# Optimization experiments

Measured on AMD Instinct MI355X. Metric: run time of the kernel, lower is better.

## Reference

```python
import jax, jax.numpy as jnp
import numpy as np

N, E, H = 100000, 3200000, 128


def setup_inputs() -> dict:
    key = jax.random.key(0)
    ks = jax.random.split(key, 12)
    s = 1.0 / np.sqrt(H)
    x = jax.random.normal(ks[0], (N, H), dtype=jnp.float32)
    edge_index = jax.random.randint(ks[1], (2, E), 0, N, dtype=jnp.int64)
    # GatedGraphConv weight: [num_layers=1, H, H] -> single [H, H]
    W = jax.random.normal(ks[2], (H, H), dtype=jnp.float32) * s
    # GRUCell (gate order: r, z, n)
    gru_w_ih = jax.random.normal(ks[3], (3 * H, H), dtype=jnp.float32) * s
    gru_w_hh = jax.random.normal(ks[4], (3 * H, H), dtype=jnp.float32) * s
    gru_b_ih = jax.random.normal(ks[5], (3 * H,), dtype=jnp.float32) * s
    gru_b_hh = jax.random.normal(ks[6], (3 * H,), dtype=jnp.float32) * s
    # LSTM layer 0 (gate order: i, f, g, o)
    lstm_w_ih = jax.random.normal(ks[7], (4 * H, H), dtype=jnp.float32) * s
    lstm_w_hh = jax.random.normal(ks[8], (4 * H, H), dtype=jnp.float32) * s
    lstm_b_ih = jax.random.normal(ks[9], (4 * H,), dtype=jnp.float32) * s
    lstm_b_hh = jax.random.normal(ks[10], (4 * H,), dtype=jnp.float32) * s
    return {
        "x": x, "edge_index": edge_index, "W": W,
        "gru_w_ih": gru_w_ih, "gru_w_hh": gru_w_hh,
        "gru_b_ih": gru_b_ih, "gru_b_hh": gru_b_hh,
        "lstm_w_ih": lstm_w_ih, "lstm_w_hh": lstm_w_hh,
        "lstm_b_ih": lstm_b_ih, "lstm_b_hh": lstm_b_hh,
    }


def _forward(x, edge_index, W, gru_w_ih, gru_w_hh, gru_b_ih, gru_b_hh,
             lstm_w_ih, lstm_w_hh, lstm_b_ih, lstm_b_hh):
    n = x.shape[0]
    src, dst = edge_index[0], edge_index[1]
    # GatedGraphConv, num_layers=1, mean aggregation
    m = x @ W                                   # [N, H]
    msg = m[src]                                # [E, H] gather (memory-bound)
    agg_sum = jax.ops.segment_sum(msg, dst, num_segments=n)
    deg = jax.ops.segment_sum(jnp.ones((src.shape[0],), x.dtype), dst, num_segments=n)
    agg = agg_sum / jnp.maximum(deg, 1.0)[:, None]
    # GRUCell(agg, x): gates r, z, n
    gi = agg @ gru_w_ih.T + gru_b_ih
    gh = x @ gru_w_hh.T + gru_b_hh
    i_r, i_z, i_n = jnp.split(gi, 3, axis=-1)
    h_r, h_z, h_n = jnp.split(gh, 3, axis=-1)
    r = jax.nn.sigmoid(i_r + h_r)
    z = jax.nn.sigmoid(i_z + h_z)
    ng = jnp.tanh(i_n + r * h_n)
    h_conv = (1.0 - z) * ng + z * x             # conv output H_tilde
    # 1-layer LSTM over seq_len=1 with zero initial (H, C)
    gates = h_conv @ lstm_w_ih.T + lstm_b_ih + lstm_b_hh  # h0 = 0
    i_g, f_g, g_g, o_g = jnp.split(gates, 4, axis=-1)
    c = jax.nn.sigmoid(i_g) * jnp.tanh(g_g)
    h_lstm = jax.nn.sigmoid(o_g) * jnp.tanh(c)
    return jax.nn.relu(h_lstm)


def reference(x, edge_index, W, gru_w_ih, gru_w_hh, gru_b_ih, gru_b_hh,
              lstm_w_ih, lstm_w_hh, lstm_b_ih, lstm_b_hh):
    return _forward(x, edge_index, W, gru_w_ih, gru_w_hh, gru_b_ih, gru_b_hh,
                    lstm_w_ih, lstm_w_hh, lstm_b_ih, lstm_b_hh)
```

## Files before the change

kernel.cpp:

```cpp
#include <hip/hip_runtime.h>
#include <math.h>

#define HD 128
#define PB 256
#define SCB 4096

typedef __attribute__((ext_vector_type(8))) short short8;
typedef __attribute__((ext_vector_type(4))) float f32x4;

__device__ __forceinline__ float sigf(float v) { return 1.0f / (1.0f + __expf(-v)); }

__device__ __forceinline__ unsigned short f2bf(float f) {
  union { float f; unsigned u; } v; v.f = f;
  unsigned r = (v.u + 0x7fffu + ((v.u >> 16) & 1u)) >> 16;
  return (unsigned short)r;
}
__device__ __forceinline__ float bf2f(unsigned short b) {
  union { unsigned u; float f; } v; v.u = ((unsigned)b) << 16;
  return v.f;
}


__global__ __launch_bounds__(256) void bcount_k(const int* __restrict__ ei,
                                                int* __restrict__ bcnt,
                                                int E, int N, int shift, int NB) {
  __shared__ int h[256];
  const int blk = blockIdx.x, tid = threadIdx.x;
  h[tid] = 0;
  __syncthreads();
  int per = (E + PB - 1) / PB;
  int lo = blk * per;
  int hi = (lo + per < E) ? lo + per : E;
  for (int e = lo + tid; e < hi; e += 256) {
    int d = ei[(size_t)E + e];
    if ((unsigned)d >= (unsigned)N) continue;
    atomicAdd(&h[d >> shift], 1);
  }
  __syncthreads();
  if (tid < NB) bcnt[tid * PB + blk] = h[tid];
}

__global__ __launch_bounds__(256) void scan1_k(const int* __restrict__ a,
                                               int* __restrict__ bsums, int total) {
  __shared__ int ts[256];
  int b = blockIdx.x, tid = threadIdx.x;
  int lo = b * SCB + tid * 16;
  int s = 0;
#pragma unroll
  for (int i = 0; i < 16; ++i) {
    int idx = lo + i;
    if (idx < total) s += a[idx];
  }
  ts[tid] = s;
  __syncthreads();
  for (int off = 128; off > 0; off >>= 1) {
    if (tid < off) ts[tid] += ts[tid + off];
    __syncthreads();
  }
  if (tid == 0) bsums[b] = ts[0];
}

__global__ __launch_bounds__(256) void scan2_k(int* __restrict__ bsums, int nb) {
  __shared__ int ts[256];
  int tid = threadIdx.x;
  int v = (tid < nb) ? bsums[tid] : 0;
  ts[tid] = v;
  __syncthreads();
  for (int off = 1; off < 256; off <<= 1) {
    int u = (tid >= off) ? ts[tid - off] : 0;
    __syncthreads();
    ts[tid] += u;
    __syncthreads();
  }
  if (tid < nb) bsums[tid] = ts[tid] - v;
}

__global__ __launch_bounds__(256) void scan3_k(int* __restrict__ a,
                                               const int* __restrict__ bsums,
                                               int total, int nblk) {
  __shared__ int ts[256];
  int b = blockIdx.x, tid = threadIdx.x;
  int lo = b * SCB + tid * 16;
  int pre[16];
  int s = 0;
#pragma unroll
  for (int i = 0; i < 16; ++i) {
    int idx = lo + i;
    int xv = (idx < total) ? a[idx] : 0;
    pre[i] = s;
    s += xv;
  }
  ts[tid] = s;
  __syncthreads();
  for (int off = 1; off < 256; off <<= 1) {
    int u = (tid >= off) ? ts[tid - off] : 0;
    __syncthreads();
    ts[tid] += u;
    __syncthreads();
  }
  int off0 = ts[tid] - s + bsums[b];
#pragma unroll
  for (int i = 0; i < 16; ++i) {
    int idx = lo + i;
    if (idx < total) a[idx] = off0 + pre[i];
  }
  if (b == nblk - 1 && tid == 255) a[total] = off0 + s;
}

__global__ __launch_bounds__(256) void bpart_k(const int* __restrict__ ei,
                                               const int* __restrict__ bstart,
                                               unsigned* __restrict__ ebuf,
                                               int E, int N, int shift, int NB,
                                               int sbits) {
  __shared__ int cur[256];
  const int blk = blockIdx.x, tid = threadIdx.x;
  if (tid < NB) cur[tid] = bstart[tid * PB + blk];
  __syncthreads();
  int per = (E + PB - 1) / PB;
  int lo = blk * per;
  int hi = (lo + per < E) ? lo + per : E;
  const unsigned dmask = (1u << shift) - 1u;
  for (int e = lo + tid; e < hi; e += 256) {
    int s = ei[e];
    int d = ei[(size_t)E + e];
    if ((unsigned)s >= (unsigned)N || (unsigned)d >= (unsigned)N) continue;
    int p = atomicAdd(&cur[d >> shift], 1);
    ebuf[p] = (((unsigned)d & dmask) << sbits) | (unsigned)s;
  }
}

__global__ __launch_bounds__(256) void bfill2_k(const unsigned* __restrict__ ebuf,
                                                const int* __restrict__ bstart,
                                                int* __restrict__ rowstart,
                                                int* __restrict__ csr,
                                                int N, int shift, int NB, int sbits) {
  __shared__ int cnt[2048];
  __shared__ int tsum[256];
  const int b = blockIdx.x, tid = threadIdx.x;
  const int d0 = b << shift;
  int dmax = d0 + (1 << shift);
  if (dmax > N) dmax = N;
  const int nd = dmax - d0;
  const unsigned smask = (1u << sbits) - 1u;
  for (int i = tid; i < nd; i += 256) cnt[i] = 0;
  __syncthreads();
  const int base = bstart[b * PB];
  const int end = bstart[(b + 1) * PB];
  for (int idx = base + tid; idx < end; idx += 256)
    atomicAdd(&cnt[ebuf[idx] >> sbits], 1);
  __syncthreads();
  const int C = (nd + 255) / 256;
  int lo = tid * C;
  int hi = (lo + C < nd) ? lo + C : nd;
  int loc[8];
  int s = 0;
  for (int i = lo; i < hi; ++i) {
    loc[i - lo] = cnt[i];
    s += cnt[i];
  }
  tsum[tid] = s;
  __syncthreads();
  for (int off = 1; off < 256; off <<= 1) {
    int u = (tid >= off) ? tsum[tid - off] : 0;
    __syncthreads();
    tsum[tid] += u;
    __syncthreads();
  }
  int run = tsum[tid] - s + base;
  for (int i = lo; i < hi; ++i) {
    rowstart[d0 + i] = run;
    cnt[i] = run;
    run += loc[i - lo];
  }
  if (b == NB - 1 && tid == 255) rowstart[N] = end;
  __syncthreads();
  for (int idx = base + tid; idx < end; idx += 256) {
    unsigned pk = ebuf[idx];
    int p = atomicAdd(&cnt[pk >> sbits], 1);
    csr[p] = (int)(pk & smask);
  }
}


__global__ __launch_bounds__(256) void convx_k(const float* __restrict__ x,
                                               unsigned short* __restrict__ xb, int n4) {
  int t = blockIdx.x * 256 + threadIdx.x;
  if (t >= n4) return;
  float4 v = reinterpret_cast<const float4*>(x)[t];
  ushort4 o;
  o.x = f2bf(v.x); o.y = f2bf(v.y); o.z = f2bf(v.z); o.w = f2bf(v.w);
  reinterpret_cast<ushort4*>(xb)[t] = o;
}

__global__ __launch_bounds__(256) void prepw_k(
    const float* __restrict__ gwhh, const float* __restrict__ lwih,
    const float* __restrict__ lbih, const float* __restrict__ lbhh,
    unsigned short* __restrict__ gwhhb, unsigned short* __restrict__ lwb,
    float* __restrict__ lbias) {
  int t = blockIdx.x * 256 + threadIdx.x;
  if (t < 49152) { gwhhb[t] = f2bf(gwhh[t]); return; }
  t -= 49152;
  if (t < 49152) {
    int j = t >> 7, k = t & 127;
    int jm = j < 128 ? j : j + 128;
    lwb[t] = f2bf(lwih[(size_t)jm * 128 + k]);
    return;
  }
  t -= 49152;
  if (t < 384) {
    int jm = t < 128 ? t : t + 128;
    lbias[t] = lbih[jm] + lbhh[jm];
  }
}

__global__ __launch_bounds__(256) void prepbp_k(const float* __restrict__ W,
                                                const float* __restrict__ gwih,
                                                unsigned short* __restrict__ Bpb) {
  int t = blockIdx.x * 256 + threadIdx.x;
  if (t >= 49152) return;
  int j = t >> 7, k = t & 127;
  const float4* wr = reinterpret_cast<const float4*>(W + (size_t)k * 128);
  const float4* gr = reinterpret_cast<const float4*>(gwih + (size_t)j * 128);
  float acc = 0.f;
#pragma unroll
  for (int c = 0; c < 32; ++c) {
    float4 a = wr[c], b = gr[c];
    acc += a.x * b.x + a.y * b.y + a.z * b.z + a.w * b.w;
  }
  Bpb[t] = f2bf(acc);
}

__device__ __forceinline__ void acc8(float* acc, uint4 v) {
  acc[0] += bf2f((unsigned short)v.x);
  acc[1] += bf2f((unsigned short)(v.x >> 16));
  acc[2] += bf2f((unsigned short)v.y);
  acc[3] += bf2f((unsigned short)(v.y >> 16));
  acc[4] += bf2f((unsigned short)v.z);
  acc[5] += bf2f((unsigned short)(v.z >> 16));
  acc[6] += bf2f((unsigned short)v.w);
  acc[7] += bf2f((unsigned short)(v.w >> 16));
}

__global__ __launch_bounds__(256) void gather_b_k(const int* __restrict__ csr,
                                                  const int* __restrict__ rowstart,
                                                  const unsigned short* __restrict__ xb,
                                                  unsigned short* __restrict__ xaggb, int N) {
  int w = (int)(((long long)blockIdx.x * 256 + threadIdx.x) >> 6);
  if (w >= N) return;
  const int lane = threadIdx.x & 63;
  const int sub = lane >> 4, li = lane & 15;
  const int beg = rowstart[w], end = rowstart[w + 1];
  const uint4* x4 = reinterpret_cast<const uint4*>(xb);

  float acc[8] = {0.f, 0.f, 0.f, 0.f, 0.f, 0.f, 0.f, 0.f};

  int j = beg;
  for (; j + 16 <= end; j += 16) {
    int s0 = csr[j + sub];
    int s1 = csr[j + 4 + sub];
    int s2 = csr[j + 8 + sub];
    int s3 = csr[j + 12 + sub];
    uint4 v0 = x4[(size_t)s0 * 16 + li];
    uint4 v1 = x4[(size_t)s1 * 16 + li];
    uint4 v2 = x4[(size_t)s2 * 16 + li];
    uint4 v3 = x4[(size_t)s3 * 16 + li];
    acc8(acc, v0); acc8(acc, v1); acc8(acc, v2); acc8(acc, v3);
  }
  for (; j + 4 <= end; j += 4) {
    int s0 = csr[j + sub];
    uint4 v0 = x4[(size_t)s0 * 16 + li];
    acc8(acc, v0);
  }
  int rem = end - j;
  if (sub < rem) {
    int s0 = csr[j + sub];
    uint4 v0 = x4[(size_t)s0 * 16 + li];
    acc8(acc, v0);
  }

#pragma unroll
  for (int i = 0; i < 8; ++i) {
    acc[i] += __shfl_xor(acc[i], 16, 64);
    acc[i] += __shfl_xor(acc[i], 32, 64);
  }

  if (lane < 16) {
    float scale = 1.0f / fmaxf((float)(end - beg), 1.0f);
    uint4 o;
    o.x = (unsigned)f2bf(acc[0] * scale) | ((unsigned)f2bf(acc[1] * scale) << 16);
    o.y = (unsigned)f2bf(acc[2] * scale) | ((unsigned)f2bf(acc[3] * scale) << 16);
    o.z = (unsigned)f2bf(acc[4] * scale) | ((unsigned)f2bf(acc[5] * scale) << 16);
    o.w = (unsigned)f2bf(acc[6] * scale) | ((unsigned)f2bf(acc[7] * scale) << 16);
    reinterpret_cast<uint4*>(xaggb)[(size_t)w * 16 + li] = o;
  }
}

__global__ __launch_bounds__(256) void gru_fused_k(
    const unsigned short* __restrict__ xaggb, const unsigned short* __restrict__ xb,
    const unsigned short* __restrict__ Bpb, const unsigned short* __restrict__ gwhhb,
    const float* __restrict__ gbih, const float* __restrict__ gbhh,
    unsigned short* __restrict__ hconv, int nrows) {
  __shared__ unsigned short Bsm[6][32][136];
  const int tid = threadIdx.x;
  const int w = tid >> 6, lane = tid & 63;
  const int q = lane >> 4, r = lane & 15;
  const int row0 = blockIdx.y * 64;
  const int c0 = blockIdx.x * 32;

#pragma unroll
  for (int it = 0; it < 12; ++it) {
    int idx = it * 256 + tid;
    int p = idx >> 9;
    int rem = idx & 511;
    int col = rem >> 4, kq = rem & 15;
    const unsigned short* src =
        (p < 3) ? Bpb + ((size_t)(p * 128 + c0 + col)) * HD
                : gwhhb + ((size_t)((p - 3) * 128 + c0 + col)) * HD;
    uint4 v = *reinterpret_cast<const uint4*>(src + kq * 8);
    *reinterpret_cast<uint4*>(&Bsm[p][col][kq * 8]) = v;
  }
  __syncthreads();

  int arow = row0 + (w << 4) + r;
  int ar = arow < nrows ? arow : nrows - 1;
  const unsigned short* Aa = xaggb + (size_t)ar * HD + q * 8;
  const unsigned short* Ax = xb + (size_t)ar * HD + q * 8;

  f32x4 acc[6][2];
#pragma unroll
  for (int p = 0; p < 6; ++p)
#pragma unroll
    for (int cb = 0; cb < 2; ++cb) acc[p][cb] = (f32x4)0.f;

#pragma unroll
  for (int ks = 0; ks < 4; ++ks) {
    short8 a1 = *reinterpret_cast<const short8*>(Aa + ks * 32);
    short8 a2 = *reinterpret_cast<const short8*>(Ax + ks * 32);
#pragma unroll
    for (int p = 0; p < 6; ++p) {
      short8 af = (p < 3) ? a1 : a2;
#pragma unroll
      for (int cb = 0; cb < 2; ++cb) {
        short8 bf = *reinterpret_cast<const short8*>(&Bsm[p][cb * 16 + r][ks * 32 + q * 8]);
        acc[p][cb] = __builtin_amdgcn_mfma_f32_16x16x32_bf16(af, bf, acc[p][cb], 0, 0, 0);
      }
    }
  }

#pragma unroll
  for (int cb = 0; cb < 2; ++cb) {
    int col = c0 + cb * 16 + r;
    float bir = gbih[col], biz = gbih[col + 128], bin = gbih[col + 256];
    float bhr = gbhh[col], bhz = gbhh[col + 128], bhn = gbhh[col + 256];
#pragma unroll
    for (int reg = 0; reg < 4; ++reg) {
      int row = row0 + (w << 4) + q * 4 + reg;
      if (row < nrows) {
        float ir = acc[0][cb][reg] + bir, iz = acc[1][cb][reg] + biz;
        float inn = acc[2][cb][reg] + bin;
        float hr = acc[3][cb][reg] + bhr, hz = acc[4][cb][reg] + bhz;
        float hn = acc[5][cb][reg] + bhn;
        float rr = sigf(ir + hr), zz = sigf(iz + hz);
        float nn = tanhf(inn + rr * hn);
        float xv = bf2f(xb[(size_t)row * HD + col]);
        hconv[(size_t)row * HD + col] = f2bf((1.f - zz) * nn + zz * xv);
      }
    }
  }
}

__global__ __launch_bounds__(256) void lstm_fused_k(
    const unsigned short* __restrict__ hconv, const unsigned short* __restrict__ lwb,
    const float* __restrict__ lbias, float* __restrict__ out, int nrows) {
  __shared__ unsigned short Bsm[3][64][136];
  const int tid = threadIdx.x;
  const int w = tid >> 6, lane = tid & 63;
  const int q = lane >> 4, r = lane & 15;
  const int row0 = blockIdx.y * 64;
  const int c0 = blockIdx.x * 64;

#pragma unroll
  for (int it = 0; it < 12; ++it) {
    int idx = it * 256 + tid;
    int p = idx >> 10, rem = idx & 1023;
    int col = rem >> 4, kq = rem & 15;
    uint4 v = *reinterpret_cast<const uint4*>(
        lwb + ((size_t)(p * 128 + c0 + col)) * HD + kq * 8);
    *reinterpret_cast<uint4*>(&Bsm[p][col][kq * 8]) = v;
  }
  __syncthreads();

  int arow = row0 + (w << 4) + r;
  int ar = arow < nrows ? arow : nrows - 1;
  const unsigned short* Ap = hconv + (size_t)ar * HD + q * 8;

  f32x4 acc[3][4];
#pragma unroll
  for (int p = 0; p < 3; ++p)
#pragma unroll
    for (int cb = 0; cb < 4; ++cb) acc[p][cb] = (f32x4)0.f;

#pragma unroll
  for (int ks = 0; ks < 4; ++ks) {
    short8 af = *reinterpret_cast<const short8*>(Ap + ks * 32);
#pragma unroll
    for (int p = 0; p < 3; ++p)
#pragma unroll
      for (int cb = 0; cb < 4; ++cb) {
        short8 bf = *reinterpret_cast<const short8*>(&Bsm[p][cb * 16 + r][ks * 32 + q * 8]);
        acc[p][cb] = __builtin_amdgcn_mfma_f32_16x16x32_bf16(af, bf, acc[p][cb], 0, 0, 0);
      }
  }

#pragma unroll
  for (int cb = 0; cb < 4; ++cb) {
    int col = c0 + cb * 16 + r;
    float bi = lbias[col], bg = lbias[col + 128], bo = lbias[col + 256];
#pragma unroll
    for (int reg = 0; reg < 4; ++reg) {
      int row = row0 + (w << 4) + q * 4 + reg;
      if (row < nrows) {
        float ig = acc[0][cb][reg] + bi;
        float gg = acc[1][cb][reg] + bg;
        float og = acc[2][cb][reg] + bo;
        float cc = sigf(ig) * tanhf(gg);
        out[(size_t)row * HD + col] = fmaxf(sigf(og) * tanhf(cc), 0.f);
      }
    }
  }
}


extern "C" void kernel_launch(void* const* d_in, const int* in_sizes, int n_in,
                              void* d_out, int out_size, void* d_ws, size_t ws_size,
                              hipStream_t stream) {
  const float* x = (const float*)d_in[0];
  const int* ei = (const int*)d_in[1];
  const float* W = (const float*)d_in[2];
  const float* gw_ih = (const float*)d_in[3];
  const float* gw_hh = (const float*)d_in[4];
  const float* gb_ih = (const float*)d_in[5];
  const float* gb_hh = (const float*)d_in[6];
  const float* lw_ih = (const float*)d_in[7];
  const float* lb_ih = (const float*)d_in[9];
  const float* lb_hh = (const float*)d_in[10];
  float* out = (float*)d_out;

  const int N = in_sizes[0] / HD;
  const int E = in_sizes[1] / 2;
  const size_t nH = (size_t)N * HD;

  int shift = 9;
  while (((N + (1 << shift) - 1) >> shift) > 256) ++shift;
  const int NB = (N + (1 << shift) - 1) >> shift;
  const int sbits = 32 - shift;

  const size_t N4p = (size_t)((N + 1 + 7) & ~7);
  const size_t E4 = (size_t)((E + 3) & ~3);
  const size_t BC = (size_t)NB * PB + 8;
  const int sc_total = NB * PB;
  const int sc_nblk = (sc_total + SCB - 1) / SCB;

  char* p = (char*)d_ws;
  int* rowstart = (int*)p;  p += 4 * N4p;
  int* bcnt = (int*)p;      p += 4 * BC;
  int* bsums = (int*)p;     p += 4 * 64;
  int* csr = (int*)p;       p += 4 * E4;
  size_t sz_eb = 4 * E4, sz_xb = 2 * nH;
  unsigned* ebuf = (unsigned*)p;
  unsigned short* xb = (unsigned short*)p;
  p += (sz_eb > sz_xb ? sz_eb : sz_xb);
  unsigned short* hconv = (unsigned short*)p;  p += 2 * nH;
  unsigned short* Bpb = (unsigned short*)p;    p += 2 * 49152;
  unsigned short* gwhhb = (unsigned short*)p;  p += 2 * 49152;
  unsigned short* lwb = (unsigned short*)p;    p += 2 * 49152;
  float* lbias = (float*)p;                    p += 4 * 384;

  unsigned short* xaggb = (unsigned short*)d_out;

  dim3 blk(256);
  unsigned rb = (unsigned)((N + 63) / 64);

  bcount_k<<<PB, blk, 0, stream>>>(ei, bcnt, E, N, shift, NB);
  scan1_k<<<sc_nblk, blk, 0, stream>>>(bcnt, bsums, sc_total);
  scan2_k<<<1, blk, 0, stream>>>(bsums, sc_nblk);
  scan3_k<<<sc_nblk, blk, 0, stream>>>(bcnt, bsums, sc_total, sc_nblk);
  bpart_k<<<PB, blk, 0, stream>>>(ei, bcnt, ebuf, E, N, shift, NB, sbits);
  bfill2_k<<<NB, blk, 0, stream>>>(ebuf, bcnt, rowstart, csr, N, shift, NB, sbits);

  convx_k<<<(unsigned)((nH / 4 + 255) / 256), blk, 0, stream>>>(x, xb, (int)(nH / 4));
  prepw_k<<<(2 * 49152 + 384 + 255) / 256, blk, 0, stream>>>(
      gw_hh, lw_ih, lb_ih, lb_hh, gwhhb, lwb, lbias);
  prepbp_k<<<192, blk, 0, stream>>>(W, gw_ih, Bpb);

  long long gthreads = (long long)N * 64;
  gather_b_k<<<(unsigned)((gthreads + 255) / 256), blk, 0, stream>>>(
      csr, rowstart, xb, xaggb, N);

  gru_fused_k<<<dim3(4, rb), blk, 0, stream>>>(
      xaggb, xb, Bpb, gwhhb, gb_ih, gb_hh, hconv, N);

  lstm_fused_k<<<dim3(2, rb), blk, 0, stream>>>(hconv, lwb, lbias, out, N);
}
```

Measured before the change: 500.2 us.

## Make GRU/LSTM GEMM kernels persistent and merge prep kernels into one launch

The GRU and LSTM fused GEMM kernels become persistent grid-stride loops over row tiles, with a capped grid of 512 blocks each. Each block loads its weight slice into shared memory and its biases once, then reuses them across many tiles instead of reloading them for every 64-row tile. The three preprocessing kernels (x conversion to bf16, weight conversion, and the W·W_ih product) are merged into a single launch to cut launch overhead. The trade-off is fewer blocks in flight, which may reduce the latency hiding available for the memory-bound A-row loads.

```diff
diff --git a/kernel.cpp b/kernel.cpp
--- a/kernel.cpp
+++ b/kernel.cpp
@@ -181,23 +181,22 @@
   }
 }
 
-
-__global__ __launch_bounds__(256) void convx_k(const float* __restrict__ x,
-                                               unsigned short* __restrict__ xb, int n4) {
-  int t = blockIdx.x * 256 + threadIdx.x;
-  if (t >= n4) return;
-  float4 v = reinterpret_cast<const float4*>(x)[t];
-  ushort4 o;
-  o.x = f2bf(v.x); o.y = f2bf(v.y); o.z = f2bf(v.z); o.w = f2bf(v.w);
-  reinterpret_cast<ushort4*>(xb)[t] = o;
-}
-
-__global__ __launch_bounds__(256) void prepw_k(
+__global__ __launch_bounds__(256) void prep_all_k(
+    const float* __restrict__ x, unsigned short* __restrict__ xb, int n4,
     const float* __restrict__ gwhh, const float* __restrict__ lwih,
     const float* __restrict__ lbih, const float* __restrict__ lbhh,
+    const float* __restrict__ W, const float* __restrict__ gwih,
     unsigned short* __restrict__ gwhhb, unsigned short* __restrict__ lwb,
-    float* __restrict__ lbias) {
+    float* __restrict__ lbias, unsigned short* __restrict__ Bpb) {
   int t = blockIdx.x * 256 + threadIdx.x;
+  if (t < n4) {
+    float4 v = reinterpret_cast<const float4*>(x)[t];
+    ushort4 o;
+    o.x = f2bf(v.x); o.y = f2bf(v.y); o.z = f2bf(v.z); o.w = f2bf(v.w);
+    reinterpret_cast<ushort4*>(xb)[t] = o;
+    return;
+  }
+  t -= n4;
   if (t < 49152) { gwhhb[t] = f2bf(gwhh[t]); return; }
   t -= 49152;
   if (t < 49152) {
@@ -210,24 +209,21 @@
   if (t < 384) {
     int jm = t < 128 ? t : t + 128;
     lbias[t] = lbih[jm] + lbhh[jm];
-  }
-}
-
-__global__ __launch_bounds__(256) void prepbp_k(const float* __restrict__ W,
-                                                const float* __restrict__ gwih,
-                                                unsigned short* __restrict__ Bpb) {
-  int t = blockIdx.x * 256 + threadIdx.x;
-  if (t >= 49152) return;
-  int j = t >> 7, k = t & 127;
-  const float4* wr = reinterpret_cast<const float4*>(W + (size_t)k * 128);
-  const float4* gr = reinterpret_cast<const float4*>(gwih + (size_t)j * 128);
-  float acc = 0.f;
-#pragma unroll
-  for (int c = 0; c < 32; ++c) {
-    float4 a = wr[c], b = gr[c];
-    acc += a.x * b.x + a.y * b.y + a.z * b.z + a.w * b.w;
-  }
-  Bpb[t] = f2bf(acc);
+    return;
+  }
+  t -= 384;
+  if (t < 49152) {
+    int j = t >> 7, k = t & 127;
+    const float4* wr = reinterpret_cast<const float4*>(W + (size_t)k * 128);
+    const float4* gr = reinterpret_cast<const float4*>(gwih + (size_t)j * 128);
+    float acc = 0.f;
+#pragma unroll
+    for (int c = 0; c < 32; ++c) {
+      float4 a = wr[c], b = gr[c];
+      acc += a.x * b.x + a.y * b.y + a.z * b.z + a.w * b.w;
+    }
+    Bpb[t] = f2bf(acc);
+  }
 }
 
 __device__ __forceinline__ void acc8(float* acc, uint4 v) {
@@ -304,7 +300,6 @@
   const int tid = threadIdx.x;
   const int w = tid >> 6, lane = tid & 63;
   const int q = lane >> 4, r = lane & 15;
-  const int row0 = blockIdx.y * 64;
   const int c0 = blockIdx.x * 32;
 
 #pragma unroll
@@ -321,49 +316,59 @@
   }
   __syncthreads();
 
-  int arow = row0 + (w << 4) + r;
-  int ar = arow < nrows ? arow : nrows - 1;
-  const unsigned short* Aa = xaggb + (size_t)ar * HD + q * 8;
-  const unsigned short* Ax = xb + (size_t)ar * HD + q * 8;
-
-  f32x4 acc[6][2];
-#pragma unroll
-  for (int p = 0; p < 6; ++p)
-#pragma unroll
-    for (int cb = 0; cb < 2; ++cb) acc[p][cb] = (f32x4)0.f;
-
-#pragma unroll
-  for (int ks = 0; ks < 4; ++ks) {
-    short8 a1 = *reinterpret_cast<const short8*>(Aa + ks * 32);
-    short8 a2 = *reinterpret_cast<const short8*>(Ax + ks * 32);
-#pragma unroll
-    for (int p = 0; p < 6; ++p) {
-      short8 af = (p < 3) ? a1 : a2;
-#pragma unroll
-      for (int cb = 0; cb < 2; ++cb) {
-        short8 bf = *reinterpret_cast<const short8*>(&Bsm[p][cb * 16 + r][ks * 32 + q * 8]);
-        acc[p][cb] = __builtin_amdgcn_mfma_f32_16x16x32_bf16(af, bf, acc[p][cb], 0, 0, 0);
+  float bir[2], biz[2], bin[2], bhr[2], bhz[2], bhn[2];
+#pragma unroll
+  for (int cb = 0; cb < 2; ++cb) {
+    int col = c0 + cb * 16 + r;
+    bir[cb] = gbih[col]; biz[cb] = gbih[col + 128]; bin[cb] = gbih[col + 256];
+    bhr[cb] = gbhh[col]; bhz[cb] = gbhh[col + 128]; bhn[cb] = gbhh[col + 256];
+  }
+
+  const int ntiles = (nrows + 63) >> 6;
+  for (int tile = blockIdx.y; tile < ntiles; tile += gridDim.y) {
+    const int row0 = tile << 6;
+    int arow = row0 + (w << 4) + r;
+    int ar = arow < nrows ? arow : nrows - 1;
+    const unsigned short* Aa = xaggb + (size_t)ar * HD + q * 8;
+    const unsigned short* Ax = xb + (size_t)ar * HD + q * 8;
+
+    f32x4 acc[6][2];
+#pragma unroll
+    for (int p = 0; p < 6; ++p)
+#pragma unroll
+      for (int cb = 0; cb < 2; ++cb) acc[p][cb] = (f32x4)0.f;
+
+#pragma unroll
+    for (int ks = 0; ks < 4; ++ks) {
+      short8 a1 = *reinterpret_cast<const short8*>(Aa + ks * 32);
+      short8 a2 = *reinterpret_cast<const short8*>(Ax + ks * 32);
+#pragma unroll
+      for (int p = 0; p < 6; ++p) {
+        short8 af = (p < 3) ? a1 : a2;
+#pragma unroll
+        for (int cb = 0; cb < 2; ++cb) {
+          short8 bf = *reinterpret_cast<const short8*>(&Bsm[p][cb * 16 + r][ks * 32 + q * 8]);
+          acc[p][cb] = __builtin_amdgcn_mfma_f32_16x16x32_bf16(af, bf, acc[p][cb], 0, 0, 0);
+        }
       }
     }
-  }
-
-#pragma unroll
-  for (int cb = 0; cb < 2; ++cb) {
-    int col = c0 + cb * 16 + r;
-    float bir = gbih[col], biz = gbih[col + 128], bin = gbih[col + 256];
-    float bhr = gbhh[col], bhz = gbhh[col + 128], bhn = gbhh[col + 256];
-#pragma unroll
-    for (int reg = 0; reg < 4; ++reg) {
-      int row = row0 + (w << 4) + q * 4 + reg;
-      if (row < nrows) {
-        float ir = acc[0][cb][reg] + bir, iz = acc[1][cb][reg] + biz;
-        float inn = acc[2][cb][reg] + bin;
-        float hr = acc[3][cb][reg] + bhr, hz = acc[4][cb][reg] + bhz;
-        float hn = acc[5][cb][reg] + bhn;
-        float rr = sigf(ir + hr), zz = sigf(iz + hz);
-        float nn = tanhf(inn + rr * hn);
-        float xv = bf2f(xb[(size_t)row * HD + col]);
-        hconv[(size_t)row * HD + col] = f2bf((1.f - zz) * nn + zz * xv);
+
+#pragma unroll
+    for (int cb = 0; cb < 2; ++cb) {
+      int col = c0 + cb * 16 + r;
+#pragma unroll
+      for (int reg = 0; reg < 4; ++reg) {
+        int row = row0 + (w << 4) + q * 4 + reg;
+        if (row < nrows) {
+          float ir = acc[0][cb][reg] + bir[cb], iz = acc[1][cb][reg] + biz[cb];
+          float inn = acc[2][cb][reg] + bin[cb];
+          float hr = acc[3][cb][reg] + bhr[cb], hz = acc[4][cb][reg] + bhz[cb];
+          float hn = acc[5][cb][reg] + bhn[cb];
+          float rr = sigf(ir + hr), zz = sigf(iz + hz);
+          float nn = tanhf(inn + rr * hn);
+          float xv = bf2f(xb[(size_t)row * HD + col]);
+          hconv[(size_t)row * HD + col] = f2bf((1.f - zz) * nn + zz * xv);
+        }
       }
     }
   }
@@ -376,7 +381,6 @@
   const int tid = threadIdx.x;
   const int w = tid >> 6, lane = tid & 63;
   const int q = lane >> 4, r = lane & 15;
-  const int row0 = blockIdx.y * 64;
   const int c0 = blockIdx.x * 64;
 
 #pragma unroll
@@ -390,41 +394,51 @@
   }
   __syncthreads();
 
-  int arow = row0 + (w << 4) + r;
-  int ar = arow < nrows ? arow : nrows - 1;
-  const unsigned short* Ap = hconv + (size_t)ar * HD + q * 8;
-
-  f32x4 acc[3][4];
-#pragma unroll
-  for (int p = 0; p < 3; ++p)
-#pragma unroll
-    for (int cb = 0; cb < 4; ++cb) acc[p][cb] = (f32x4)0.f;
-
-#pragma unroll
-  for (int ks = 0; ks < 4; ++ks) {
-    short8 af = *reinterpret_cast<const short8*>(Ap + ks * 32);
-#pragma unroll
-    for (int p = 0; p < 3; ++p)
-#pragma unroll
-      for (int cb = 0; cb < 4; ++cb) {
-        short8 bf = *reinterpret_cast<const short8*>(&Bsm[p][cb * 16 + r][ks * 32 + q * 8]);
-        acc[p][cb] = __builtin_amdgcn_mfma_f32_16x16x32_bf16(af, bf, acc[p][cb], 0, 0, 0);
-      }
-  }
-
+  float bi[4], bg[4], bo[4];
 #pragma unroll
   for (int cb = 0; cb < 4; ++cb) {
     int col = c0 + cb * 16 + r;
-    float bi = lbias[col], bg = lbias[col + 128], bo = lbias[col + 256];
-#pragma unroll
-    for (int reg = 0; reg < 4; ++reg) {
-      int row = row0 + (w << 4) + q * 4 + reg;
-      if (row < nrows) {
-        float ig = acc[0][cb][reg] + bi;
-        float gg = acc[1][cb][reg] + bg;
-        float og = acc[2][cb][reg] + bo;
-        float cc = sigf(ig) * tanhf(gg);
-        out[(size_t)row * HD + col] = fmaxf(sigf(og) * tanhf(cc), 0.f);
+    bi[cb] = lbias[col]; bg[cb] = lbias[col + 128]; bo[cb] = lbias[col + 256];
+  }
+
+  const int ntiles = (nrows + 63) >> 6;
+  for (int tile = blockIdx.y; tile < ntiles; tile += gridDim.y) {
+    const int row0 = tile << 6;
+    int arow = row0 + (w << 4) + r;
+    int ar = arow < nrows ? arow : nrows - 1;
+    const unsigned short* Ap = hconv + (size_t)ar * HD + q * 8;
+
+    f32x4 acc[3][4];
+#pragma unroll
+    for (int p = 0; p < 3; ++p)
+#pragma unroll
+      for (int cb = 0; cb < 4; ++cb) acc[p][cb] = (f32x4)0.f;
+
+#pragma unroll
+    for (int ks = 0; ks < 4; ++ks) {
+      short8 af = *reinterpret_cast<const short8*>(Ap + ks * 32);
+#pragma unroll
+      for (int p = 0; p < 3; ++p)
+#pragma unroll
+        for (int cb = 0; cb < 4; ++cb) {
+          short8 bf = *reinterpret_cast<const short8*>(&Bsm[p][cb * 16 + r][ks * 32 + q * 8]);
+          acc[p][cb] = __builtin_amdgcn_mfma_f32_16x16x32_bf16(af, bf, acc[p][cb], 0, 0, 0);
+        }
+    }
+
+#pragma unroll
+    for (int cb = 0; cb < 4; ++cb) {
+      int col = c0 + cb * 16 + r;
+#pragma unroll
+      for (int reg = 0; reg < 4; ++reg) {
+        int row = row0 + (w << 4) + q * 4 + reg;
+        if (row < nrows) {
+          float ig = acc[0][cb][reg] + bi[cb];
+          float gg = acc[1][cb][reg] + bg[cb];
+          float og = acc[2][cb][reg] + bo[cb];
+          float cc = sigf(ig) * tanhf(gg);
+          out[(size_t)row * HD + col] = fmaxf(sigf(og) * tanhf(cc), 0.f);
+        }
       }
     }
   }
@@ -479,7 +493,7 @@
   unsigned short* xaggb = (unsigned short*)d_out;
 
   dim3 blk(256);
-  unsigned rb = (unsigned)((N + 63) / 64);
+  const int ntiles = (N + 63) / 64;
 
   bcount_k<<<PB, blk, 0, stream>>>(ei, bcnt, E, N, shift, NB);
   scan1_k<<<sc_nblk, blk, 0, stream>>>(bcnt, bsums, sc_total);
@@ -488,17 +502,25 @@
   bpart_k<<<PB, blk, 0, stream>>>(ei, bcnt, ebuf, E, N, shift, NB, sbits);
   bfill2_k<<<NB, blk, 0, stream>>>(ebuf, bcnt, rowstart, csr, N, shift, NB, sbits);
 
-  convx_k<<<(unsigned)((nH / 4 + 255) / 256), blk, 0, stream>>>(x, xb, (int)(nH / 4));
-  prepw_k<<<(2 * 49152 + 384 + 255) / 256, blk, 0, stream>>>(
-      gw_hh, lw_ih, lb_ih, lb_hh, gwhhb, lwb, lbias);
-  prepbp_k<<<192, blk, 0, stream>>>(W, gw_ih, Bpb);
+  {
+    long long tthreads = (long long)(nH / 4) + 49152 + 49152 + 384 + 49152;
+    prep_all_k<<<(unsigned)((tthreads + 255) / 256), blk, 0, stream>>>(
+        x, xb, (int)(nH / 4), gw_hh, lw_ih, lb_ih, lb_hh, W, gw_ih,
+        gwhhb, lwb, lbias, Bpb);
+  }
 
   long long gthreads = (long long)N * 64;
   gather_b_k<<<(unsigned)((gthreads + 255) / 256), blk, 0, stream>>>(
       csr, rowstart, xb, xaggb, N);
 
-  gru_fused_k<<<dim3(4, rb), blk, 0, stream>>>(
-      xaggb, xb, Bpb, gwhhb, gb_ih, gb_hh, hconv, N);
-
-  lstm_fused_k<<<dim3(2, rb), blk, 0, stream>>>(hconv, lwb, lbias, out, N);
-}
+  {
+    int G = ntiles < 128 ? ntiles : 128;
+    gru_fused_k<<<dim3(4, G), blk, 0, stream>>>(
+        xaggb, xb, Bpb, gwhhb, gb_ih, gb_hh, hconv, N);
+  }
+
+  {
+    int G = ntiles < 256 ? ntiles : 256;
+    lstm_fused_k<<<dim3(2, G), blk, 0, stream>>>(hconv, lwb, lbias, out, N);
+  }
+}
```

Result: slower. 585.0 us (+17.0%).
